# Performance work log

Measured on AMD Instinct MI355X. Metric: run time of the kernel, lower is better.

Reference implementation:

```python
import jax, jax.numpy as jnp
import numpy as np

B = 32          # batch_size
S = 64          # num_subgraph
D = 8           # dim_multi_hot (module-level global in source repo)
NE = S * D      # num_edges = 512
NNODES = 1024
E = 150000      # incidence rows
IN_UNITS = [16, 32, 32]
OUT_UNITS = [32, 32, 16]


def _glorot(key, shape):
    # glorot_normal over last two dims (out, in)
    fan_out, fan_in = shape[-2], shape[-1]
    std = (2.0 / (fan_in + fan_out)) ** 0.5
    return std * jax.random.normal(key, shape, dtype=jnp.float32)


def setup_inputs() -> dict:
    key = jax.random.key(0)
    ks = jax.random.split(key, 10)
    nodes_features = jax.random.normal(ks[0], (NNODES * S, IN_UNITS[0]), dtype=jnp.float32)
    c0 = jax.random.randint(ks[1], (E,), 0, B, dtype=jnp.int32)
    c1 = jax.random.randint(ks[2], (E,), 0, NNODES, dtype=jnp.int32)
    c2 = jax.random.randint(ks[3], (E,), 0, S, dtype=jnp.int32)
    c3 = jax.random.randint(ks[4], (E,), 0, D, dtype=jnp.int32)
    incidence_matrix = jnp.stack([c0, c1, c2, c3], axis=1)
    return {
        'nodes_features': nodes_features,
        'in_core0': _glorot(ks[5], (NE, IN_UNITS[1], IN_UNITS[0])),
        'in_bias0': jnp.zeros((NE, IN_UNITS[1], 1), jnp.float32),
        'in_core1': _glorot(ks[6], (NE, IN_UNITS[2], IN_UNITS[1])),
        'in_bias1': jnp.zeros((NE, IN_UNITS[2], 1), jnp.float32),
        'out_core0': _glorot(ks[7], (NE, OUT_UNITS[1], OUT_UNITS[0])),
        'out_bias0': jnp.zeros((NE, OUT_UNITS[1], 1), jnp.float32),
        'out_core1': _glorot(ks[8], (NE, OUT_UNITS[2], OUT_UNITS[1])),
        'out_bias1': jnp.zeros((NE, OUT_UNITS[2], 1), jnp.float32),
        'incidence_matrix': incidence_matrix,
    }


def reference(nodes_features, in_core0, in_bias0, in_core1, in_bias1,
              out_core0, out_bias0, out_core1, out_bias1, incidence_matrix):
    c0 = incidence_matrix[:, 0]
    c1 = incidence_matrix[:, 1]
    c2 = incidence_matrix[:, 2]
    c3 = incidence_matrix[:, 3]

    # gather node features per incidence row: [E, in0]
    x = nodes_features[c1 * S + c2]
    eidx = c2 * D + c3  # per-edge weight index, < NE

    # per-edge MLP (gathered batched matmul + bias + relu)
    for W, b in ((in_core0, in_bias0), (in_core1, in_bias1)):
        x = jax.nn.relu(jnp.einsum('eoi,ei->eo', W[eidx], x) + b[eidx, :, 0])

    # unsorted segment mean over irregular edge groups
    seg = c0 * (D * S) + c2 * D + c3
    nseg = B * S * D
    sums = jax.ops.segment_sum(x, seg, num_segments=nseg)           # [B*NE, 32]
    cnt = jax.ops.segment_sum(jnp.ones((x.shape[0], 1), x.dtype), seg, num_segments=nseg)
    ef = jnp.where(cnt > 0, sums / jnp.maximum(cnt, 1.0), 0.0)       # [B*NE, 32]

    # output MLP: weights tiled over batch (einsum avoids explicit repeat)
    ef = ef.reshape(B, NE, -1)
    for W, b in ((out_core0, out_bias0), (out_core1, out_bias1)):
        ef = jax.nn.relu(jnp.einsum('eoi,bei->beo', W, ef) + b[None, :, :, 0])

    return ef.reshape(B * NE, OUT_UNITS[-1], 1)
```

## Files before the change

kernel.cpp:

```cpp
#include <hip/hip_runtime.h>

#define B_    32
#define S_    64
#define D_    8
#define NE_   512
#define E_    150000
#define CAP   448
#define CSTRIDE 16

#define PAYLOAD_BYTE_OFF (NE_ * CSTRIDE * 4)

typedef __attribute__((ext_vector_type(8)))  short  short8;
typedef __attribute__((ext_vector_type(16))) float  float16;

__device__ __forceinline__ unsigned short f2bf(float f) {
    union { float f; unsigned int u; } cv; cv.f = f;
    unsigned int u = cv.u;
    return (unsigned short)((u + 0x7fffu + ((u >> 16) & 1u)) >> 16);
}
__device__ __forceinline__ unsigned int pack2bf(float a, float b) {
    return (unsigned int)f2bf(a) | ((unsigned int)f2bf(b) << 16);
}

__global__ __launch_bounds__(1024)
void scatter_light(const int* __restrict__ inc,
                   int* __restrict__ cursor,
                   int* __restrict__ payload) {
    __shared__ int lcount[NE_];
    __shared__ int lbase[NE_];
    const int tid = threadIdx.x;

    for (int i = tid; i < NE_; i += 1024) lcount[i] = 0;
    __syncthreads();

    const int e = blockIdx.x * 1024 + tid;
    int ei = -1, lp = 0, pl = 0;
    if (e < E_) {
        const int4 c = ((const int4*)inc)[e];
        ei = c.z * D_ + c.w;
        pl = (c.x << 16) | (c.y * S_ + c.z);
        lp = atomicAdd(&lcount[ei], 1);
    }
    __syncthreads();
    for (int i = tid; i < NE_; i += 1024) {
        const int c = lcount[i];
        lbase[i] = (c > 0) ? atomicAdd(&cursor[i * CSTRIDE], c) : 0;
    }
    __syncthreads();
    if (ei >= 0) {
        const int idx = lbase[ei] + lp;
        if (idx < CAP) payload[ei * CAP + idx] = pl;
    }
}

#define HLP 40

__global__ __launch_bounds__(512, 4)
void main_mfma(const float* __restrict__ nf,
               const float* __restrict__ iw0, const float* __restrict__ ib0,
               const float* __restrict__ iw1, const float* __restrict__ ib1,
               const float* __restrict__ ow0, const float* __restrict__ ob0,
               const float* __restrict__ ow1, const float* __restrict__ ob1,
               const int* __restrict__ cursor, const int* __restrict__ payload,
               float* __restrict__ out) {
    const int bid  = blockIdx.x;
    const int tid  = threadIdx.x;
    const int lane = tid & 63;
    const int wav  = tid >> 6;
    const int e32  = lane & 31;
    const int q    = lane >> 5;

    __shared__ float acc[32][33];
    __shared__ float hb[32][33];
    __shared__ float cnts[32];
    __shared__ float q0t[32 * 33];
    __shared__ float q1t[32 * 17];
    __shared__ float qb0s[32], qb1s[16];
    __shared__ float bias0s[32], bias1s[32];
    __shared__ unsigned short Hl[8][32 * HLP];

    short8 aWa, aWb0, aWb1;
    {
        const float* wa = iw0 + (size_t)bid * 512 + e32 * 16 + q * 8;
        float4 u0 = ((const float4*)wa)[0], u1 = ((const float4*)wa)[1];
        unsigned int p[4] = { pack2bf(u0.x,u0.y), pack2bf(u0.z,u0.w),
                              pack2bf(u1.x,u1.y), pack2bf(u1.z,u1.w) };
        aWa = *(short8*)p;
    }
    {
        const float* wb = iw1 + (size_t)bid * 1024 + e32 * 32 + q * 8;
        float4 u0 = ((const float4*)wb)[0], u1 = ((const float4*)wb)[1];
        unsigned int p[4] = { pack2bf(u0.x,u0.y), pack2bf(u0.z,u0.w),
                              pack2bf(u1.x,u1.y), pack2bf(u1.z,u1.w) };
        aWb0 = *(short8*)p;
        const float* wb2 = wb + 16;
        float4 u2 = ((const float4*)wb2)[0], u3 = ((const float4*)wb2)[1];
        unsigned int p2[4] = { pack2bf(u2.x,u2.y), pack2bf(u2.z,u2.w),
                               pack2bf(u3.x,u3.y), pack2bf(u3.z,u3.w) };
        aWb1 = *(short8*)p2;
    }

    for (int i = tid; i < 1024; i += 512) {
        const int o = i >> 5, k = i & 31;
        q0t[k * 33 + o] = ow0[(size_t)bid * 1024 + i];
    }
    { const int o = tid >> 5, k = tid & 31;
      q1t[k * 17 + o] = ow1[(size_t)bid * 512 + tid]; }
    if (tid < 32)       { bias0s[tid] = ib0[bid * 32 + tid]; cnts[tid] = 0.f; }
    else if (tid < 64)  bias1s[tid - 32] = ib1[bid * 32 + (tid - 32)];
    else if (tid < 96)  qb0s[tid - 64] = ob0[bid * 32 + (tid - 64)];
    else if (tid < 112) qb1s[tid - 96] = ob1[bid * 16 + (tid - 96)];
    for (int i = tid; i < 32 * 33; i += 512) ((float*)acc)[i] = 0.f;
    __syncthreads();

    const int n = min(cursor[bid * CSTRIDE], CAP);
    const int ntiles = (n + 31) >> 5;
    const int* Pl = payload + bid * CAP;
    unsigned short* hl = Hl[wav];

    for (int t = wav; t < ntiles; t += 8) {
        const int slot  = t * 32 + e32;
        const bool valid = slot < n;
        const int cs    = valid ? slot : (n - 1);

        const int p   = Pl[cs];
        const int b_e = p >> 16;
        const int row = p & 0xFFFF;

        short8 bX;
        {
            const float4* xp = (const float4*)(nf + (size_t)row * 16 + q * 8);
            float4 u0 = xp[0], u1 = xp[1];
            unsigned int pk[4] = { pack2bf(u0.x,u0.y), pack2bf(u0.z,u0.w),
                                   pack2bf(u1.x,u1.y), pack2bf(u1.z,u1.w) };
            bX = *(short8*)pk;
        }

        float16 c0;
        #pragma unroll
        for (int r = 0; r < 16; ++r) {
            const int o_r = (r & 3) + 8 * (r >> 2) + 4 * q;
            c0[r] = bias0s[o_r];
        }
        c0 = __builtin_amdgcn_mfma_f32_32x32x16_bf16(aWa, bX, c0, 0, 0, 0);

        #pragma unroll
        for (int r = 0; r < 16; r += 2) {
            const int o_r = (r & 3) + 8 * (r >> 2) + 4 * q;
            const unsigned int pk = pack2bf(fmaxf(c0[r], 0.f), fmaxf(c0[r + 1], 0.f));
            *(unsigned int*)(hl + e32 * HLP + o_r) = pk;
        }

        short8 bH0 = *(const short8*)(hl + e32 * HLP + q * 8);
        short8 bH1 = *(const short8*)(hl + e32 * HLP + 16 + q * 8);
        float16 c1;
        #pragma unroll
        for (int r = 0; r < 16; ++r) {
            const int o_r = (r & 3) + 8 * (r >> 2) + 4 * q;
            c1[r] = bias1s[o_r];
        }
        c1 = __builtin_amdgcn_mfma_f32_32x32x16_bf16(aWb0, bH0, c1, 0, 0, 0);
        c1 = __builtin_amdgcn_mfma_f32_32x32x16_bf16(aWb1, bH1, c1, 0, 0, 0);

        if (valid) {
            #pragma unroll
            for (int r = 0; r < 16; ++r) {
                const int o_r = (r & 3) + 8 * (r >> 2) + 4 * q;
                atomicAdd(&acc[b_e][o_r], fmaxf(c1[r], 0.f));
            }
            if (q == 0) atomicAdd(&cnts[b_e], 1.f);
        }
    }
    __syncthreads();

    {
        const int b  = tid >> 4;
        const int j  = tid & 15;
        const float cv  = cnts[b];
        const float inv = cv > 0.f ? 1.0f / cv : 0.0f;
        #pragma unroll
        for (int s = 0; s < 2; ++s) {
            const int oo = j * 2 + s;
            float d = 0.f;
            #pragma unroll
            for (int k = 0; k < 32; ++k) d = fmaf(q0t[k * 33 + oo], acc[b][k], d);
            hb[b][oo] = fmaxf(fmaf(d, inv, qb0s[oo]), 0.f);
        }
    }
    __syncthreads();

    {
        const int b = tid >> 4;
        const int o = tid & 15;
        float d = qb1s[o];
        #pragma unroll
        for (int k = 0; k < 32; ++k) d = fmaf(q1t[k * 17 + o], hb[b][k], d);
        out[((size_t)b * NE_ + bid) * 16 + o] = fmaxf(d, 0.f);
    }
}

extern "C" void kernel_launch(void* const* d_in, const int* in_sizes, int n_in,
                              void* d_out, int out_size, void* d_ws, size_t ws_size,
                              hipStream_t stream) {
    const float* nf  = (const float*)d_in[0];
    const float* iw0 = (const float*)d_in[1];
    const float* ib0 = (const float*)d_in[2];
    const float* iw1 = (const float*)d_in[3];
    const float* ib1 = (const float*)d_in[4];
    const float* ow0 = (const float*)d_in[5];
    const float* ob0 = (const float*)d_in[6];
    const float* ow1 = (const float*)d_in[7];
    const float* ob1 = (const float*)d_in[8];
    const int*   inc = (const int*)d_in[9];

    int* cursor  = (int*)d_ws;
    int* payload = (int*)((char*)d_ws + PAYLOAD_BYTE_OFF);

    hipMemsetAsync(cursor, 0, NE_ * CSTRIDE * 4, stream);
    scatter_light<<<(E_ + 1023) / 1024, 1024, 0, stream>>>(inc, cursor, payload);
    main_mfma<<<NE_, 512, 0, stream>>>(nf, iw0, ib0, iw1, ib1, ow0, ob0, ow1, ob1,
                                       cursor, payload, (float*)d_out);
}
```

Measured before the change: 118.6 us.

## Replace global-atomic cursor binning with per-block bins and in-kernel prefix scan

```diff
diff --git a/kernel.cpp b/kernel.cpp
--- a/kernel.cpp
+++ b/kernel.cpp
@@ -6,9 +6,13 @@
 #define NE_   512
 #define E_    150000
 #define CAP   448
-#define CSTRIDE 16
-
-#define PAYLOAD_BYTE_OFF (NE_ * CSTRIDE * 4)
+
+#define SBLK  1024
+#define BLKN  ((E_ + SBLK - 1) / SBLK)
+#define SLOTS 16
+#define PBIN_PITCH (BLKN * SLOTS)
+
+#define PAYLOAD_BYTE_OFF (NE_ * BLKN * 4)
 
 typedef __attribute__((ext_vector_type(8)))  short  short8;
 typedef __attribute__((ext_vector_type(16))) float  float16;
@@ -22,18 +26,17 @@
     return (unsigned int)f2bf(a) | ((unsigned int)f2bf(b) << 16);
 }
 
-__global__ __launch_bounds__(1024)
-void scatter_light(const int* __restrict__ inc,
-                   int* __restrict__ cursor,
-                   int* __restrict__ payload) {
+__global__ __launch_bounds__(SBLK)
+void scatter_bin(const int* __restrict__ inc,
+                 int* __restrict__ cnt2D,
+                 int* __restrict__ payload2D) {
     __shared__ int lcount[NE_];
-    __shared__ int lbase[NE_];
     const int tid = threadIdx.x;
 
-    for (int i = tid; i < NE_; i += 1024) lcount[i] = 0;
-    __syncthreads();
-
-    const int e = blockIdx.x * 1024 + tid;
+    for (int i = tid; i < NE_; i += SBLK) lcount[i] = 0;
+    __syncthreads();
+
+    const int e = blockIdx.x * SBLK + tid;
     int ei = -1, lp = 0, pl = 0;
     if (e < E_) {
         const int4 c = ((const int4*)inc)[e];
@@ -41,16 +44,11 @@
         pl = (c.x << 16) | (c.y * S_ + c.z);
         lp = atomicAdd(&lcount[ei], 1);
     }
-    __syncthreads();
-    for (int i = tid; i < NE_; i += 1024) {
-        const int c = lcount[i];
-        lbase[i] = (c > 0) ? atomicAdd(&cursor[i * CSTRIDE], c) : 0;
-    }
-    __syncthreads();
-    if (ei >= 0) {
-        const int idx = lbase[ei] + lp;
-        if (idx < CAP) payload[ei * CAP + idx] = pl;
-    }
+    if (ei >= 0 && lp < SLOTS)
+        payload2D[ei * PBIN_PITCH + blockIdx.x * SLOTS + lp] = pl;
+    __syncthreads();
+    if (tid < NE_)
+        cnt2D[tid * BLKN + blockIdx.x] = min(lcount[tid], SLOTS);
 }
 
 #define HLP 40
@@ -61,7 +59,7 @@
                const float* __restrict__ iw1, const float* __restrict__ ib1,
                const float* __restrict__ ow0, const float* __restrict__ ob0,
                const float* __restrict__ ow1, const float* __restrict__ ob1,
-               const int* __restrict__ cursor, const int* __restrict__ payload,
+               const int* __restrict__ cnt2D, const int* __restrict__ payload2D,
                float* __restrict__ out) {
     const int bid  = blockIdx.x;
     const int tid  = threadIdx.x;
@@ -77,6 +75,8 @@
     __shared__ float q1t[32 * 17];
     __shared__ float qb0s[32], qb1s[16];
     __shared__ float bias0s[32], bias1s[32];
+    __shared__ int   scnt[256];
+    __shared__ int   elist[CAP];
     __shared__ unsigned short Hl[8][32 * HLP];
 
     short8 aWa, aWb0, aWb1;
@@ -100,6 +100,10 @@
         aWb1 = *(short8*)p2;
     }
 
+    int mycnt = 0;
+    if (tid < BLKN) mycnt = cnt2D[bid * BLKN + tid];
+    if (tid < 256)  scnt[tid] = (tid < BLKN) ? mycnt : 0;
+
     for (int i = tid; i < 1024; i += 512) {
         const int o = i >> 5, k = i & 31;
         q0t[k * 33 + o] = ow0[(size_t)bid * 1024 + i];
@@ -113,9 +117,29 @@
     for (int i = tid; i < 32 * 33; i += 512) ((float*)acc)[i] = 0.f;
     __syncthreads();
 
-    const int n = min(cursor[bid * CSTRIDE], CAP);
+    #pragma unroll
+    for (int off = 1; off < 256; off <<= 1) {
+        int v = 0;
+        if (tid < 256) { v = scnt[tid]; if (tid >= off) v += scnt[tid - off]; }
+        __syncthreads();
+        if (tid < 256) scnt[tid] = v;
+        __syncthreads();
+    }
+    const int n = min(scnt[BLKN - 1], CAP);
+
+    const int* Pb = payload2D + (size_t)bid * PBIN_PITCH;
+    for (int pair = tid; pair < PBIN_PITCH; pair += 512) {
+        const int blk = pair >> 4, s = pair & (SLOTS - 1);
+        const int b0 = blk ? scnt[blk - 1] : 0;
+        const int cc = scnt[blk] - b0;
+        if (s < cc) {
+            const int idx = b0 + s;
+            if (idx < CAP) elist[idx] = Pb[pair];
+        }
+    }
+    __syncthreads();
+
     const int ntiles = (n + 31) >> 5;
-    const int* Pl = payload + bid * CAP;
     unsigned short* hl = Hl[wav];
 
     for (int t = wav; t < ntiles; t += 8) {
@@ -123,7 +147,7 @@
         const bool valid = slot < n;
         const int cs    = valid ? slot : (n - 1);
 
-        const int p   = Pl[cs];
+        const int p   = elist[cs];
         const int b_e = p >> 16;
         const int row = p & 0xFFFF;
 
@@ -213,11 +237,10 @@
     const float* ob1 = (const float*)d_in[8];
     const int*   inc = (const int*)d_in[9];
 
-    int* cursor  = (int*)d_ws;
-    int* payload = (int*)((char*)d_ws + PAYLOAD_BYTE_OFF);
-
-    hipMemsetAsync(cursor, 0, NE_ * CSTRIDE * 4, stream);
-    scatter_light<<<(E_ + 1023) / 1024, 1024, 0, stream>>>(inc, cursor, payload);
+    int* cnt2D     = (int*)d_ws;
+    int* payload2D = (int*)((char*)d_ws + PAYLOAD_BYTE_OFF);
+
+    scatter_bin<<<BLKN, SBLK, 0, stream>>>(inc, cnt2D, payload2D);
     main_mfma<<<NE_, 512, 0, stream>>>(nf, iw0, ib0, iw1, ib1, ow0, ob0, ow1, ob1,
-                                       cursor, payload, (float*)d_out);
-}
+                                       cnt2D, payload2D, (float*)d_out);
+}
```

Measured after the change: 117.5 us. No clear change (-0.9%).

## Fuse bucketing into main kernel with per-block full incidence scan, two edges per block

Applied to the files above, without the earlier changes.

```diff
diff --git a/kernel.cpp b/kernel.cpp
--- a/kernel.cpp
+++ b/kernel.cpp
@@ -6,9 +6,7 @@
 #define NE_   512
 #define E_    150000
 #define CAP   448
-#define CSTRIDE 16
-
-#define PAYLOAD_BYTE_OFF (NE_ * CSTRIDE * 4)
+#define NBLK  256
 
 typedef __attribute__((ext_vector_type(8)))  short  short8;
 typedef __attribute__((ext_vector_type(16))) float  float16;
@@ -22,108 +20,106 @@
     return (unsigned int)f2bf(a) | ((unsigned int)f2bf(b) << 16);
 }
 
-__global__ __launch_bounds__(1024)
-void scatter_light(const int* __restrict__ inc,
-                   int* __restrict__ cursor,
-                   int* __restrict__ payload) {
-    __shared__ int lcount[NE_];
-    __shared__ int lbase[NE_];
-    const int tid = threadIdx.x;
-
-    for (int i = tid; i < NE_; i += 1024) lcount[i] = 0;
-    __syncthreads();
-
-    const int e = blockIdx.x * 1024 + tid;
-    int ei = -1, lp = 0, pl = 0;
-    if (e < E_) {
-        const int4 c = ((const int4*)inc)[e];
-        ei = c.z * D_ + c.w;
-        pl = (c.x << 16) | (c.y * S_ + c.z);
-        lp = atomicAdd(&lcount[ei], 1);
-    }
-    __syncthreads();
-    for (int i = tid; i < NE_; i += 1024) {
-        const int c = lcount[i];
-        lbase[i] = (c > 0) ? atomicAdd(&cursor[i * CSTRIDE], c) : 0;
-    }
-    __syncthreads();
-    if (ei >= 0) {
-        const int idx = lbase[ei] + lp;
-        if (idx < CAP) payload[ei * CAP + idx] = pl;
-    }
-}
-
-#define HLP 40
-
-__global__ __launch_bounds__(512, 4)
-void main_mfma(const float* __restrict__ nf,
-               const float* __restrict__ iw0, const float* __restrict__ ib0,
-               const float* __restrict__ iw1, const float* __restrict__ ib1,
-               const float* __restrict__ ow0, const float* __restrict__ ob0,
-               const float* __restrict__ ow1, const float* __restrict__ ob1,
-               const int* __restrict__ cursor, const int* __restrict__ payload,
-               float* __restrict__ out) {
+struct Smem {
+    int   lcnt[2];
+    int   elist[2][CAP];
+    float acc[2][32][33];
+    float hb[2][32][33];
+    float cnts[2][32];
+    float q0t[2][32 * 33];
+    float q1t[2][32 * 17];
+    float qb0s[2][32], qb1s[2][16];
+    float bias0s[2][32], bias1s[2][32];
+};
+
+__global__ __launch_bounds__(512, 2)
+void fused_scan(const float* __restrict__ nf,
+                const float* __restrict__ iw0, const float* __restrict__ ib0,
+                const float* __restrict__ iw1, const float* __restrict__ ib1,
+                const float* __restrict__ ow0, const float* __restrict__ ob0,
+                const float* __restrict__ ow1, const float* __restrict__ ob1,
+                const int* __restrict__ inc,
+                float* __restrict__ out) {
+    __shared__ Smem s;
     const int bid  = blockIdx.x;
     const int tid  = threadIdx.x;
     const int lane = tid & 63;
     const int wav  = tid >> 6;
     const int e32  = lane & 31;
     const int q    = lane >> 5;
-
-    __shared__ float acc[32][33];
-    __shared__ float hb[32][33];
-    __shared__ float cnts[32];
-    __shared__ float q0t[32 * 33];
-    __shared__ float q1t[32 * 17];
-    __shared__ float qb0s[32], qb1s[16];
-    __shared__ float bias0s[32], bias1s[32];
-    __shared__ unsigned short Hl[8][32 * HLP];
-
-    short8 aWa, aWb0, aWb1;
-    {
-        const float* wa = iw0 + (size_t)bid * 512 + e32 * 16 + q * 8;
+    const int eA   = bid * 2;
+
+    if (tid < 2) s.lcnt[tid] = 0;
+    if (tid < 64) s.cnts[tid >> 5][tid & 31] = 0.f;
+    for (int i = tid; i < 2 * 32 * 33; i += 512) ((float*)s.acc)[i] = 0.f;
+    __syncthreads();
+
+    short8 aWa0, aWa1, aWb00, aWb01, aWb10, aWb11;
+    #pragma unroll
+    for (int sub = 0; sub < 2; ++sub) {
+        const float* wa = iw0 + (size_t)(eA + sub) * 512 + e32 * 16 + q * 8;
         float4 u0 = ((const float4*)wa)[0], u1 = ((const float4*)wa)[1];
         unsigned int p[4] = { pack2bf(u0.x,u0.y), pack2bf(u0.z,u0.w),
                               pack2bf(u1.x,u1.y), pack2bf(u1.z,u1.w) };
-        aWa = *(short8*)p;
-    }
-    {
-        const float* wb = iw1 + (size_t)bid * 1024 + e32 * 32 + q * 8;
-        float4 u0 = ((const float4*)wb)[0], u1 = ((const float4*)wb)[1];
-        unsigned int p[4] = { pack2bf(u0.x,u0.y), pack2bf(u0.z,u0.w),
-                              pack2bf(u1.x,u1.y), pack2bf(u1.z,u1.w) };
-        aWb0 = *(short8*)p;
+        if (sub == 0) aWa0 = *(short8*)p; else aWa1 = *(short8*)p;
+
+        const float* wb = iw1 + (size_t)(eA + sub) * 1024 + e32 * 32 + q * 8;
+        float4 v0 = ((const float4*)wb)[0], v1 = ((const float4*)wb)[1];
+        unsigned int p1[4] = { pack2bf(v0.x,v0.y), pack2bf(v0.z,v0.w),
+                               pack2bf(v1.x,v1.y), pack2bf(v1.z,v1.w) };
         const float* wb2 = wb + 16;
-        float4 u2 = ((const float4*)wb2)[0], u3 = ((const float4*)wb2)[1];
-        unsigned int p2[4] = { pack2bf(u2.x,u2.y), pack2bf(u2.z,u2.w),
-                               pack2bf(u3.x,u3.y), pack2bf(u3.z,u3.w) };
-        aWb1 = *(short8*)p2;
-    }
-
+        float4 v2 = ((const float4*)wb2)[0], v3 = ((const float4*)wb2)[1];
+        unsigned int p2[4] = { pack2bf(v2.x,v2.y), pack2bf(v2.z,v2.w),
+                               pack2bf(v3.x,v3.y), pack2bf(v3.z,v3.w) };
+        if (sub == 0) { aWb00 = *(short8*)p1; aWb01 = *(short8*)p2; }
+        else          { aWb10 = *(short8*)p1; aWb11 = *(short8*)p2; }
+    }
+
+    for (int i = tid; i < 2048; i += 512) {
+        const int sub = i >> 10, r = i & 1023;
+        s.q0t[sub][(r & 31) * 33 + (r >> 5)] = ow0[(size_t)(eA + sub) * 1024 + r];
+    }
     for (int i = tid; i < 1024; i += 512) {
-        const int o = i >> 5, k = i & 31;
-        q0t[k * 33 + o] = ow0[(size_t)bid * 1024 + i];
-    }
-    { const int o = tid >> 5, k = tid & 31;
-      q1t[k * 17 + o] = ow1[(size_t)bid * 512 + tid]; }
-    if (tid < 32)       { bias0s[tid] = ib0[bid * 32 + tid]; cnts[tid] = 0.f; }
-    else if (tid < 64)  bias1s[tid - 32] = ib1[bid * 32 + (tid - 32)];
-    else if (tid < 96)  qb0s[tid - 64] = ob0[bid * 32 + (tid - 64)];
-    else if (tid < 112) qb1s[tid - 96] = ob1[bid * 16 + (tid - 96)];
-    for (int i = tid; i < 32 * 33; i += 512) ((float*)acc)[i] = 0.f;
-    __syncthreads();
-
-    const int n = min(cursor[bid * CSTRIDE], CAP);
-    const int ntiles = (n + 31) >> 5;
-    const int* Pl = payload + bid * CAP;
-    unsigned short* hl = Hl[wav];
-
-    for (int t = wav; t < ntiles; t += 8) {
-        const int slot  = t * 32 + e32;
+        const int sub = i >> 9, r = i & 511;
+        s.q1t[sub][(r & 31) * 17 + (r >> 5)] = ow1[(size_t)(eA + sub) * 512 + r];
+    }
+    if (tid < 64)        s.bias0s[tid >> 5][tid & 31] = ib0[(eA + (tid >> 5)) * 32 + (tid & 31)];
+    else if (tid < 128) { const int t = tid - 64;  s.bias1s[t >> 5][t & 31] = ib1[(eA + (t >> 5)) * 32 + (t & 31)]; }
+    else if (tid < 192) { const int t = tid - 128; s.qb0s[t >> 5][t & 31]   = ob0[(eA + (t >> 5)) * 32 + (t & 31)]; }
+    else if (tid < 224) { const int t = tid - 192; s.qb1s[t >> 4][t & 15]   = ob1[(eA + (t >> 4)) * 16 + (t & 15)]; }
+
+    for (int i = tid; i < E_; i += 512) {
+        const int4 c = ((const int4*)inc)[i];
+        const int ei = c.z * D_ + c.w;
+        if ((ei >> 1) == bid) {
+            const int sub = ei & 1;
+            const int pos = atomicAdd(&s.lcnt[sub], 1);
+            if (pos < CAP) s.elist[sub][pos] = (c.x << 16) | (c.y * S_ + c.z);
+        }
+    }
+    __syncthreads();
+
+    float bA0[16], bA1[16], bB0[16], bB1[16];
+    #pragma unroll
+    for (int r = 0; r < 16; ++r) {
+        const int o_r = (r & 3) + 8 * (r >> 2) + 4 * q;
+        bA0[r] = s.bias0s[0][o_r]; bA1[r] = s.bias0s[1][o_r];
+        bB0[r] = s.bias1s[0][o_r]; bB1[r] = s.bias1s[1][o_r];
+    }
+
+    const int nA = min(s.lcnt[0], CAP), nB = min(s.lcnt[1], CAP);
+    const int tA = (nA + 31) >> 5;
+    const int tT = tA + ((nB + 31) >> 5);
+
+    for (int t = wav; t < tT; t += 8) {
+        const int  bin  = (t >= tA) ? 1 : 0;
+        const int  tt   = bin ? (t - tA) : t;
+        const int  n    = bin ? nB : nA;
+        const int  slot = tt * 32 + e32;
         const bool valid = slot < n;
-        const int cs    = valid ? slot : (n - 1);
-
-        const int p   = Pl[cs];
+        const int  cs   = valid ? slot : (n - 1);
+
+        const int p   = s.elist[bin][cs];
         const int b_e = p >> 16;
         const int row = p & 0xFFFF;
 
@@ -136,29 +132,34 @@
             bX = *(short8*)pk;
         }
 
+        const short8 aWa  = bin ? aWa1  : aWa0;
+        const short8 aWb0 = bin ? aWb10 : aWb00;
+        const short8 aWb1 = bin ? aWb11 : aWb01;
+
         float16 c0;
         #pragma unroll
-        for (int r = 0; r < 16; ++r) {
-            const int o_r = (r & 3) + 8 * (r >> 2) + 4 * q;
-            c0[r] = bias0s[o_r];
-        }
+        for (int r = 0; r < 16; ++r) c0[r] = bin ? bA1[r] : bA0[r];
         c0 = __builtin_amdgcn_mfma_f32_32x32x16_bf16(aWa, bX, c0, 0, 0, 0);
 
-        #pragma unroll
-        for (int r = 0; r < 16; r += 2) {
-            const int o_r = (r & 3) + 8 * (r >> 2) + 4 * q;
-            const unsigned int pk = pack2bf(fmaxf(c0[r], 0.f), fmaxf(c0[r + 1], 0.f));
-            *(unsigned int*)(hl + e32 * HLP + o_r) = pk;
-        }
-
-        short8 bH0 = *(const short8*)(hl + e32 * HLP + q * 8);
-        short8 bH1 = *(const short8*)(hl + e32 * HLP + 16 + q * 8);
+        float v[16];
+        #pragma unroll
+        for (int r = 0; r < 16; ++r) v[r] = fmaxf(c0[r], 0.f);
+        unsigned int A0 = pack2bf(v[0], v[1]),  B0 = pack2bf(v[2], v[3]);
+        unsigned int C0 = pack2bf(v[4], v[5]),  D0 = pack2bf(v[6], v[7]);
+        unsigned int A1 = pack2bf(v[8], v[9]),  B1 = pack2bf(v[10], v[11]);
+        unsigned int C1 = pack2bf(v[12], v[13]), D1 = pack2bf(v[14], v[15]);
+        unsigned int g0 = __shfl_xor(q ? A0 : C0, 32, 64);
+        unsigned int g1 = __shfl_xor(q ? B0 : D0, 32, 64);
+        unsigned int g2 = __shfl_xor(q ? A1 : C1, 32, 64);
+        unsigned int g3 = __shfl_xor(q ? B1 : D1, 32, 64);
+        unsigned int f0[4] = { q ? g0 : A0, q ? g1 : B0, q ? C0 : g0, q ? D0 : g1 };
+        unsigned int f1[4] = { q ? g2 : A1, q ? g3 : B1, q ? C1 : g2, q ? D1 : g3 };
+        short8 bH0 = *(short8*)f0;
+        short8 bH1 = *(short8*)f1;
+
         float16 c1;
         #pragma unroll
-        for (int r = 0; r < 16; ++r) {
-            const int o_r = (r & 3) + 8 * (r >> 2) + 4 * q;
-            c1[r] = bias1s[o_r];
-        }
+        for (int r = 0; r < 16; ++r) c1[r] = bin ? bB1[r] : bB0[r];
         c1 = __builtin_amdgcn_mfma_f32_32x32x16_bf16(aWb0, bH0, c1, 0, 0, 0);
         c1 = __builtin_amdgcn_mfma_f32_32x32x16_bf16(aWb1, bH1, c1, 0, 0, 0);
 
@@ -166,36 +167,38 @@
             #pragma unroll
             for (int r = 0; r < 16; ++r) {
                 const int o_r = (r & 3) + 8 * (r >> 2) + 4 * q;
-                atomicAdd(&acc[b_e][o_r], fmaxf(c1[r], 0.f));
+                atomicAdd(&s.acc[bin][b_e][o_r], fmaxf(c1[r], 0.f));
             }
-            if (q == 0) atomicAdd(&cnts[b_e], 1.f);
-        }
-    }
-    __syncthreads();
-
-    {
-        const int b  = tid >> 4;
-        const int j  = tid & 15;
-        const float cv  = cnts[b];
+            if (q == 0) atomicAdd(&s.cnts[bin][b_e], 1.f);
+        }
+    }
+    __syncthreads();
+
+    #pragma unroll
+    for (int sub = 0; sub < 2; ++sub) {
+        const int b = tid >> 4;
+        const int j = tid & 15;
+        const float cv  = s.cnts[sub][b];
         const float inv = cv > 0.f ? 1.0f / cv : 0.0f;
         #pragma unroll
-        for (int s = 0; s < 2; ++s) {
-            const int oo = j * 2 + s;
+        for (int t2 = 0; t2 < 2; ++t2) {
+            const int oo = j * 2 + t2;
             float d = 0.f;
             #pragma unroll
-            for (int k = 0; k < 32; ++k) d = fmaf(q0t[k * 33 + oo], acc[b][k], d);
-            hb[b][oo] = fmaxf(fmaf(d, inv, qb0s[oo]), 0.f);
-        }
-    }
-    __syncthreads();
-
-    {
+            for (int k = 0; k < 32; ++k) d = fmaf(s.q0t[sub][k * 33 + oo], s.acc[sub][b][k], d);
+            s.hb[sub][b][oo] = fmaxf(fmaf(d, inv, s.qb0s[sub][oo]), 0.f);
+        }
+    }
+    __syncthreads();
+
+    #pragma unroll
+    for (int sub = 0; sub < 2; ++sub) {
         const int b = tid >> 4;
         const int o = tid & 15;
-        float d = qb1s[o];
-        #pragma unroll
-        for (int k = 0; k < 32; ++k) d = fmaf(q1t[k * 17 + o], hb[b][k], d);
-        out[((size_t)b * NE_ + bid) * 16 + o] = fmaxf(d, 0.f);
+        float d = s.qb1s[sub][o];
+        #pragma unroll
+        for (int k = 0; k < 32; ++k) d = fmaf(s.q1t[sub][k * 17 + o], s.hb[sub][b][k], d);
+        out[((size_t)b * NE_ + eA + sub) * 16 + o] = fmaxf(d, 0.f);
     }
 }
 
@@ -213,11 +216,6 @@
     const float* ob1 = (const float*)d_in[8];
     const int*   inc = (const int*)d_in[9];
 
-    int* cursor  = (int*)d_ws;
-    int* payload = (int*)((char*)d_ws + PAYLOAD_BYTE_OFF);
-
-    hipMemsetAsync(cursor, 0, NE_ * CSTRIDE * 4, stream);
-    scatter_light<<<(E_ + 1023) / 1024, 1024, 0, stream>>>(inc, cursor, payload);
-    main_mfma<<<NE_, 512, 0, stream>>>(nf, iw0, ib0, iw1, ib1, ow0, ob0, ow1, ob1,
-                                       cursor, payload, (float*)d_out);
-}
+    fused_scan<<<NBLK, 512, 0, stream>>>(nf, iw0, ib0, iw1, ib1,
+                                         ow0, ob0, ow1, ob1, inc, (float*)d_out);
+}
```

Measured after the change: 193.3 us. +63.0%, slower.
